# Performance work log

Measured on AMD Instinct MI355X. Metric: run time of the kernel, lower is better.

Reference implementation:

```python
import jax, jax.numpy as jnp
import numpy as np

N_NODES = 50000
N_EDGES = 400000
NODE_DIM = 128
EDGE_DIM = 64
MSG_DIM = 128
EPS = 1e-5


def _linear_init(key, out_f, in_f):
    kw, kb = jax.random.split(key)
    bound = 1.0 / np.sqrt(in_f)
    W = jax.random.uniform(kw, (out_f, in_f), jnp.float32, -bound, bound)
    b = jax.random.uniform(kb, (out_f,), jnp.float32, -bound, bound)
    return W, b


def setup_inputs() -> dict:
    key = jax.random.key(0)
    ks = jax.random.split(key, 10)
    node_features = jax.random.normal(ks[0], (N_NODES, NODE_DIM), jnp.float32)
    edge_features = jax.random.normal(ks[1], (N_EDGES, EDGE_DIM), jnp.float32)
    edge_indices = jax.random.randint(ks[2], (2, N_EDGES), 0, N_NODES, jnp.int64 if jax.config.jax_enable_x64 else jnp.int32)
    cat_dim = 2 * NODE_DIM + EDGE_DIM  # 320
    Wm1, bm1 = _linear_init(ks[3], MSG_DIM, cat_dim)
    Wm2, bm2 = _linear_init(ks[4], MSG_DIM, MSG_DIM)
    Wm3, bm3 = _linear_init(ks[5], MSG_DIM, MSG_DIM)
    We1, be1 = _linear_init(ks[6], EDGE_DIM, cat_dim)
    We2, be2 = _linear_init(ks[7], EDGE_DIM, EDGE_DIM)
    Wn, bn = _linear_init(ks[8], NODE_DIM, NODE_DIM + MSG_DIM)
    gamma = jnp.ones((NODE_DIM,), jnp.float32)
    beta = jnp.zeros((NODE_DIM,), jnp.float32)
    return {
        'node_features': node_features,
        'edge_features': edge_features,
        'edge_indices': edge_indices,
        'Wm1': Wm1, 'bm1': bm1, 'Wm2': Wm2, 'bm2': bm2, 'Wm3': Wm3, 'bm3': bm3,
        'We1': We1, 'be1': be1, 'We2': We2, 'be2': be2,
        'Wn': Wn, 'bn': bn, 'gamma': gamma, 'beta': beta,
    }


def reference(node_features, edge_features, edge_indices,
              Wm1, bm1, Wm2, bm2, Wm3, bm3,
              We1, be1, We2, be2,
              Wn, bn, gamma, beta):
    src, dst = edge_indices[0], edge_indices[1]
    # [E, 2*node_dim + edge_dim]: gathered endpoints + edge feature
    h = jnp.concatenate([node_features[src], node_features[dst], edge_features], axis=-1)
    # message MLP: Linear-ReLU-Linear-ReLU-Linear
    m = jax.nn.relu(h @ Wm1.T + bm1)
    m = jax.nn.relu(m @ Wm2.T + bm2)
    m = m @ Wm3.T + bm3  # [E, msg_dim]
    # scatter-add messages to destination nodes
    messages = jax.ops.segment_sum(m, dst, num_segments=node_features.shape[0])
    # edge update MLP: Linear-ReLU-Linear
    e = jax.nn.relu(h @ We1.T + be1)
    updated_edges = e @ We2.T + be2
    # node update: Linear-ReLU-LayerNorm
    u = jax.nn.relu(jnp.concatenate([node_features, messages], axis=-1) @ Wn.T + bn)
    mu = jnp.mean(u, axis=-1, keepdims=True)
    var = jnp.mean(jnp.square(u - mu), axis=-1, keepdims=True)
    updated_nodes = (u - mu) * jax.lax.rsqrt(var + EPS) * gamma + beta
    return updated_nodes, updated_edges
```

## Files before the change

### kernel.cpp

```cpp
#include <hip/hip_runtime.h>

#define N_EDGES 400000
#define N_NODES 50000
#define ND 128
#define ED 64
#define MD 128
#define CAT 320
#define ET 64
#define MPITCH 136
#define EPITCH 72
#define H2PITCH 264

typedef unsigned short u16;
typedef __attribute__((ext_vector_type(8))) short bf16x8;
typedef __attribute__((ext_vector_type(4))) float f32x4;

#define WS_WM1 0
#define WS_WM2 40960
#define WS_WM3 57344
#define WS_WE1 73728
#define WS_WE2 94208
#define WS_WN  98304
#define WS_WEND 131072
#define WS_NFB 131072
#define WS_FULL_BYTES (2u * (WS_NFB + N_NODES * ND))

__device__ __forceinline__ u16 f2bf(float f) {
  unsigned int x = __float_as_uint(f);
  unsigned int r = (x + 0x7fffu + ((x >> 16) & 1u)) >> 16;
  return (u16)r;
}
__device__ __forceinline__ bf16x8 ld8f(const float* p) {
  f32x4 a = *(const f32x4*)p;
  f32x4 b = *(const f32x4*)(p + 4);
  bf16x8 r;
  r[0] = (short)f2bf(a[0]); r[1] = (short)f2bf(a[1]);
  r[2] = (short)f2bf(a[2]); r[3] = (short)f2bf(a[3]);
  r[4] = (short)f2bf(b[0]); r[5] = (short)f2bf(b[1]);
  r[6] = (short)f2bf(b[2]); r[7] = (short)f2bf(b[3]);
  return r;
}
template<bool WB>
__device__ __forceinline__ bf16x8 ldw(const void* w, size_t off) {
  if (WB) return *(const bf16x8*)((const u16*)w + off);
  else    return ld8f((const float*)w + off);
}
__device__ __forceinline__ int clampi(int v, int hi) {
  v = v < 0 ? 0 : v;
  return v >= hi ? hi - 1 : v;
}

__global__ __launch_bounds__(256) void prep_weights(
    const float* __restrict__ Wm1, const float* __restrict__ Wm2,
    const float* __restrict__ Wm3, const float* __restrict__ We1,
    const float* __restrict__ We2, const float* __restrict__ Wn,
    u16* __restrict__ ws)
{
  int i = blockIdx.x * 256 + threadIdx.x;
  if (i >= WS_WEND) return;
  const float* s; int off;
  if      (i < WS_WM2) { s = Wm1; off = WS_WM1; }
  else if (i < WS_WM3) { s = Wm2; off = WS_WM2; }
  else if (i < WS_WE1) { s = Wm3; off = WS_WM3; }
  else if (i < WS_WE2) { s = We1; off = WS_WE1; }
  else if (i < WS_WN)  { s = We2; off = WS_WE2; }
  else                 { s = Wn;  off = WS_WN;  }
  ws[i] = f2bf(s[i - off]);
}

__global__ __launch_bounds__(256) void prep_nf(
    const float* __restrict__ nf, u16* __restrict__ nfb)
{
  size_t t = ((size_t)blockIdx.x * 256 + threadIdx.x) * 8;
  if (t >= (size_t)N_NODES * ND) return;
  *(bf16x8*)(nfb + t) = ld8f(nf + t);
}

__device__ __forceinline__ void load_indices(
    int* sIdx, int* sFlag, const void* idxRaw, int eb, int tid)
{
  if (tid < ET) {
    unsigned w = ((const unsigned*)idxRaw)[2u * (unsigned)(eb + tid) + 1u];
    int any32 = __any(w != 0u);
    if (tid == 0) *sFlag = any32;
  }
  __syncthreads();
  const bool is32 = (*sFlag != 0);
  if (tid < ET) {
    int v = is32 ? ((const int*)idxRaw)[eb + tid]
                 : (int)((const long long*)idxRaw)[eb + tid];
    sIdx[tid] = clampi(v, N_NODES);
  } else if (tid < 2 * ET) {
    int t = tid - ET;
    int v = is32 ? ((const int*)idxRaw)[N_EDGES + eb + t]
                 : (int)((const long long*)idxRaw)[(size_t)N_EDGES + eb + t];
    sIdx[tid] = clampi(v, N_NODES);
  }
  __syncthreads();
}

template<bool WB, bool NB>
__global__ __launch_bounds__(256, 4) void edge_fused_kernel(
    const float* __restrict__ nf, const u16* __restrict__ nfb,
    const float* __restrict__ ef, const void* __restrict__ idxRaw,
    const void* __restrict__ wm1, const float* __restrict__ bm1,
    const void* __restrict__ wm2, const float* __restrict__ bm2,
    const void* __restrict__ wm3, const float* __restrict__ bm3,
    const void* __restrict__ we1, const float* __restrict__ be1,
    const void* __restrict__ we2, const float* __restrict__ be2,
    float* __restrict__ msg, float* __restrict__ outE)
{
  __shared__ __align__(16) u16 sH[ET * 256];
  __shared__ int sIdx[2 * ET];
  __shared__ int sFlag;
  u16* sM = sH;
  u16* sE1 = sH + ET * MPITCH;

  const int tid  = threadIdx.x;
  const int lane = tid & 63;
  const int wave = tid >> 6;
  const int l15  = lane & 15;
  const int quad = lane >> 4;
  const int eb   = blockIdx.x * ET;

  load_indices(sIdx, &sFlag, idxRaw, eb, tid);

#pragma unroll
  for (int i = 0; i < 8; ++i) {
    int g = i * 256 + tid;
    int e = g >> 5;
    int c = g & 31;
    int node = sIdx[(c < 16) ? e : (ET + e)];
    int cc = c & 15;
    bf16x8 v;
    if (NB) v = *(const bf16x8*)(nfb + (size_t)node * ND + cc * 8);
    else    v = ld8f(nf + (size_t)node * ND + cc * 8);
    int pc = c ^ (e & 7);
    *(bf16x8*)&sH[e * 256 + pc * 8] = v;
  }
  __syncthreads();

  f32x4 acc1[3][4] = {};
  for (int kk = 0; kk < 10; ++kk) {
    int ko = kk * 32 + quad * 8;
    bf16x8 a[4];
#pragma unroll
    for (int m = 0; m < 4; ++m) {
      int e = m * 16 + l15;
      if (kk < 8) {
        int cc = ko >> 3;
        a[m] = *(const bf16x8*)&sH[e * 256 + ((cc ^ (e & 7)) * 8)];
      } else {
        a[m] = ld8f(ef + (size_t)(eb + e) * ED + (ko - 256));
      }
    }
#pragma unroll
    for (int i = 0; i < 3; ++i) {
      int nt = 3 * wave + i;
      int f = nt * 16 + l15;
      bf16x8 b = (nt < 8) ? ldw<WB>(wm1, (size_t)f * CAT + ko)
                          : ldw<WB>(we1, (size_t)(f - ND) * CAT + ko);
#pragma unroll
      for (int m = 0; m < 4; ++m)
        acc1[i][m] = __builtin_amdgcn_mfma_f32_16x16x32_bf16(a[m], b, acc1[i][m], 0, 0, 0);
    }
  }
  __syncthreads();

#pragma unroll
  for (int i = 0; i < 3; ++i) {
    int nt = 3 * wave + i;
    int f = nt * 16 + l15;
    float bias = (nt < 8) ? bm1[f] : be1[f - ND];
#pragma unroll
    for (int m = 0; m < 4; ++m)
#pragma unroll
      for (int r = 0; r < 4; ++r) {
        int row = m * 16 + quad * 4 + r;
        float v = acc1[i][m][r] + bias;
        v = v > 0.f ? v : 0.f;
        if (nt < 8) sM[row * MPITCH + f] = f2bf(v);
        else        sE1[row * EPITCH + (f - ND)] = f2bf(v);
      }
  }
  __syncthreads();

  {
    f32x4 acc[4] = {};
    const int f = wave * 16 + l15;
    for (int kk = 0; kk < 2; ++kk) {
      int ko = kk * 32 + quad * 8;
      bf16x8 b = ldw<WB>(we2, (size_t)f * ED + ko);
#pragma unroll
      for (int m = 0; m < 4; ++m) {
        bf16x8 a = *(const bf16x8*)&sE1[(m * 16 + l15) * EPITCH + ko];
        acc[m] = __builtin_amdgcn_mfma_f32_16x16x32_bf16(a, b, acc[m], 0, 0, 0);
      }
    }
    float bias = be2[f];
#pragma unroll
    for (int m = 0; m < 4; ++m)
#pragma unroll
      for (int r = 0; r < 4; ++r) {
        int row = m * 16 + quad * 4 + r;
        outE[(size_t)(eb + row) * ED + f] = acc[m][r] + bias;
      }
  }

  f32x4 acc2[2][4] = {};
  for (int kk = 0; kk < 4; ++kk) {
    int ko = kk * 32 + quad * 8;
    bf16x8 a[4];
#pragma unroll
    for (int m = 0; m < 4; ++m)
      a[m] = *(const bf16x8*)&sM[(m * 16 + l15) * MPITCH + ko];
#pragma unroll
    for (int i = 0; i < 2; ++i) {
      int f = (2 * wave + i) * 16 + l15;
      bf16x8 b = ldw<WB>(wm2, (size_t)f * MD + ko);
#pragma unroll
      for (int m = 0; m < 4; ++m)
        acc2[i][m] = __builtin_amdgcn_mfma_f32_16x16x32_bf16(a[m], b, acc2[i][m], 0, 0, 0);
    }
  }
  __syncthreads();

#pragma unroll
  for (int i = 0; i < 2; ++i) {
    int f = (2 * wave + i) * 16 + l15;
    float bias = bm2[f];
#pragma unroll
    for (int m = 0; m < 4; ++m)
#pragma unroll
      for (int r = 0; r < 4; ++r) {
        int row = m * 16 + quad * 4 + r;
        float v = acc2[i][m][r] + bias;
        sM[row * MPITCH + f] = f2bf(v > 0.f ? v : 0.f);
      }
  }
  __syncthreads();

  f32x4 acc3[2][4] = {};
  for (int kk = 0; kk < 4; ++kk) {
    int ko = kk * 32 + quad * 8;
    bf16x8 a[4];
#pragma unroll
    for (int m = 0; m < 4; ++m)
      a[m] = *(const bf16x8*)&sM[(m * 16 + l15) * MPITCH + ko];
#pragma unroll
    for (int i = 0; i < 2; ++i) {
      int f = (2 * wave + i) * 16 + l15;
      bf16x8 b = ldw<WB>(wm3, (size_t)f * MD + ko);
#pragma unroll
      for (int m = 0; m < 4; ++m)
        acc3[i][m] = __builtin_amdgcn_mfma_f32_16x16x32_bf16(a[m], b, acc3[i][m], 0, 0, 0);
    }
  }
#pragma unroll
  for (int i = 0; i < 2; ++i) {
    int f = (2 * wave + i) * 16 + l15;
    float bias = bm3[f];
#pragma unroll
    for (int m = 0; m < 4; ++m)
#pragma unroll
      for (int r = 0; r < 4; ++r) {
        int row = m * 16 + quad * 4 + r;
        int d = sIdx[ET + row];
        atomicAdd(&msg[(size_t)d * MD + f], acc3[i][m][r] + bias);
      }
  }
}

template<bool WB, bool NB>
__global__ __launch_bounds__(256, 4) void node_kernel(
    const float* __restrict__ nf, const u16* __restrict__ nfb,
    const float* __restrict__ msg,
    const void* __restrict__ wn, const float* __restrict__ bn,
    const float* __restrict__ gamma, const float* __restrict__ beta,
    float* __restrict__ outN)
{
  __shared__ __align__(16) u16 sH[ET * H2PITCH];
  __shared__ float sPart[4][ET][2];

  const int tid  = threadIdx.x;
  const int lane = tid & 63;
  const int wave = tid >> 6;
  const int l15  = lane & 15;
  const int quad = lane >> 4;
  const int nb   = blockIdx.x * ET;

#pragma unroll
  for (int i = 0; i < 8; ++i) {
    int g = i * 256 + tid;
    int r = g >> 5;
    int c = g & 31;
    int node = nb + r;
    bool valid = node < N_NODES;
    bf16x8 v = {};
    if (c < 16) {
      if (valid) {
        if (NB) v = *(const bf16x8*)(nfb + (size_t)node * ND + c * 8);
        else    v = ld8f(nf + (size_t)node * ND + c * 8);
      }
      *(bf16x8*)&sH[r * H2PITCH + c * 8] = v;
    } else {
      int co = (c - 16) * 8;
      if (valid) v = ld8f(msg + (size_t)node * MD + co);
      *(bf16x8*)&sH[r * H2PITCH + ND + co] = v;
    }
  }
  __syncthreads();

  f32x4 acc[2][4] = {};
  for (int kk = 0; kk < 8; ++kk) {
    int ko = kk * 32 + quad * 8;
    bf16x8 a[4];
#pragma unroll
    for (int m = 0; m < 4; ++m)
      a[m] = *(const bf16x8*)&sH[(m * 16 + l15) * H2PITCH + ko];
#pragma unroll
    for (int i = 0; i < 2; ++i) {
      int f = (2 * wave + i) * 16 + l15;
      bf16x8 b = ldw<WB>(wn, (size_t)f * 256 + ko);
#pragma unroll
      for (int m = 0; m < 4; ++m)
        acc[i][m] = __builtin_amdgcn_mfma_f32_16x16x32_bf16(a[m], b, acc[i][m], 0, 0, 0);
    }
  }

#pragma unroll
  for (int i = 0; i < 2; ++i) {
    int f = (2 * wave + i) * 16 + l15;
    float bias = bn[f];
#pragma unroll
    for (int m = 0; m < 4; ++m)
#pragma unroll
      for (int r = 0; r < 4; ++r) {
        float v = acc[i][m][r] + bias;
        acc[i][m][r] = v > 0.f ? v : 0.f;
      }
  }

#pragma unroll
  for (int m = 0; m < 4; ++m)
#pragma unroll
    for (int r = 0; r < 4; ++r) {
      float p = acc[0][m][r] + acc[1][m][r];
      float q = acc[0][m][r] * acc[0][m][r] + acc[1][m][r] * acc[1][m][r];
#pragma unroll
      for (int mk = 1; mk < 16; mk <<= 1) {
        p += __shfl_xor(p, mk);
        q += __shfl_xor(q, mk);
      }
      if (l15 == 0) {
        int row = m * 16 + quad * 4 + r;
        sPart[wave][row][0] = p;
        sPart[wave][row][1] = q;
      }
    }
  __syncthreads();

#pragma unroll
  for (int m = 0; m < 4; ++m)
#pragma unroll
    for (int r = 0; r < 4; ++r) {
      int row = m * 16 + quad * 4 + r;
      float ts  = sPart[0][row][0] + sPart[1][row][0] + sPart[2][row][0] + sPart[3][row][0];
      float tss = sPart[0][row][1] + sPart[1][row][1] + sPart[2][row][1] + sPart[3][row][1];
      float mu  = ts * 0.0078125f;
      float var = tss * 0.0078125f - mu * mu;
      var = var > 0.f ? var : 0.f;
      float rstd = rsqrtf(var + 1e-5f);
      int node = nb + row;
      if (node < N_NODES) {
#pragma unroll
        for (int i = 0; i < 2; ++i) {
          int f = (2 * wave + i) * 16 + l15;
          float o = (acc[i][m][r] - mu) * rstd * gamma[f] + beta[f];
          outN[(size_t)node * ND + f] = o;
        }
      }
    }
}

extern "C" void kernel_launch(void* const* d_in, const int* in_sizes, int n_in,
                              void* d_out, int out_size, void* d_ws, size_t ws_size,
                              hipStream_t stream)
{
  const float* nf  = (const float*)d_in[0];
  const float* ef  = (const float*)d_in[1];
  const void*  ei  = d_in[2];
  const float* Wm1 = (const float*)d_in[3];
  const float* bm1 = (const float*)d_in[4];
  const float* Wm2 = (const float*)d_in[5];
  const float* bm2 = (const float*)d_in[6];
  const float* Wm3 = (const float*)d_in[7];
  const float* bm3 = (const float*)d_in[8];
  const float* We1 = (const float*)d_in[9];
  const float* be1 = (const float*)d_in[10];
  const float* We2 = (const float*)d_in[11];
  const float* be2 = (const float*)d_in[12];
  const float* Wn  = (const float*)d_in[13];
  const float* bn  = (const float*)d_in[14];
  const float* gamma = (const float*)d_in[15];
  const float* beta  = (const float*)d_in[16];

  float* outN = (float*)d_out;
  float* outE = outN + (size_t)N_NODES * ND;
  float* msg  = outN;

  const bool haveW  = ws_size >= (size_t)(2u * WS_WEND);
  const bool haveNF = ws_size >= (size_t)WS_FULL_BYTES;
  u16* ws = (u16*)d_ws;
  const u16* nfb = ws + WS_NFB;

  hipMemsetAsync(msg, 0, (size_t)N_NODES * MD * sizeof(float), stream);

  if (haveW) {
    prep_weights<<<(WS_WEND + 255) / 256, 256, 0, stream>>>(
        Wm1, Wm2, Wm3, We1, We2, Wn, ws);
    if (haveNF)
      prep_nf<<<(N_NODES * ND / 8 + 255) / 256, 256, 0, stream>>>(nf, ws + WS_NFB);
  }

  const int egrid = N_EDGES / ET;
  const int ngrid = (N_NODES + ET - 1) / ET;

  if (haveW && haveNF) {
    edge_fused_kernel<true, true><<<egrid, 256, 0, stream>>>(
        nf, nfb, ef, ei,
        ws + WS_WM1, bm1, ws + WS_WM2, bm2, ws + WS_WM3, bm3,
        ws + WS_WE1, be1, ws + WS_WE2, be2, msg, outE);
    node_kernel<true, true><<<ngrid, 256, 0, stream>>>(
        nf, nfb, msg, ws + WS_WN, bn, gamma, beta, outN);
  } else if (haveW) {
    edge_fused_kernel<true, false><<<egrid, 256, 0, stream>>>(
        nf, nullptr, ef, ei,
        ws + WS_WM1, bm1, ws + WS_WM2, bm2, ws + WS_WM3, bm3,
        ws + WS_WE1, be1, ws + WS_WE2, be2, msg, outE);
    node_kernel<true, false><<<ngrid, 256, 0, stream>>>(
        nf, nullptr, msg, ws + WS_WN, bn, gamma, beta, outN);
  } else {
    edge_fused_kernel<false, false><<<egrid, 256, 0, stream>>>(
        nf, nullptr, ef, ei,
        Wm1, bm1, Wm2, bm2, Wm3, bm3, We1, be1, We2, be2, msg, outE);
    node_kernel<false, false><<<ngrid, 256, 0, stream>>>(
        nf, nullptr, msg, Wn, bn, gamma, beta, outN);
  }
}
```

Measured before the change: 532.8 us.

## Drop shared index staging and barriers in edge kernel, shrink node tile

In the edge kernel, edge indices are now read straight from global memory per thread rather than staged in shared memory, which removes two barriers and the shared index arrays. The index-width detection now uses only the first 64 entries, read by each wave. The edge kernel's occupancy hint rises from 4 to 5 blocks per CU. The node kernel moves to 32-node tiles with an occupancy hint of 6, giving more blocks and less shared memory per block. The risks are redundant global index loads, register spills under the tighter launch bounds, and weights reloaded across twice as many node blocks.

```diff
diff --git a/kernel.cpp b/kernel.cpp
--- a/kernel.cpp
+++ b/kernel.cpp
@@ -7,6 +7,7 @@
 #define MD 128
 #define CAT 320
 #define ET 64
+#define NT 32
 #define MPITCH 136
 #define EPITCH 72
 #define H2PITCH 264
@@ -48,6 +49,14 @@
 __device__ __forceinline__ int clampi(int v, int hi) {
   v = v < 0 ? 0 : v;
   return v >= hi ? hi - 1 : v;
+}
+__device__ __forceinline__ bool detect32(const void* idxRaw, int lane) {
+  unsigned w = ((const unsigned*)idxRaw)[2 * lane + 1];
+  return __any(w != 0u) != 0;
+}
+__device__ __forceinline__ int ldidx(const void* idxRaw, bool is32, size_t pos) {
+  return is32 ? ((const int*)idxRaw)[pos]
+              : (int)((const long long*)idxRaw)[pos];
 }
 
 __global__ __launch_bounds__(256) void prep_weights(
@@ -76,31 +85,8 @@
   *(bf16x8*)(nfb + t) = ld8f(nf + t);
 }
 
-__device__ __forceinline__ void load_indices(
-    int* sIdx, int* sFlag, const void* idxRaw, int eb, int tid)
-{
-  if (tid < ET) {
-    unsigned w = ((const unsigned*)idxRaw)[2u * (unsigned)(eb + tid) + 1u];
-    int any32 = __any(w != 0u);
-    if (tid == 0) *sFlag = any32;
-  }
-  __syncthreads();
-  const bool is32 = (*sFlag != 0);
-  if (tid < ET) {
-    int v = is32 ? ((const int*)idxRaw)[eb + tid]
-                 : (int)((const long long*)idxRaw)[eb + tid];
-    sIdx[tid] = clampi(v, N_NODES);
-  } else if (tid < 2 * ET) {
-    int t = tid - ET;
-    int v = is32 ? ((const int*)idxRaw)[N_EDGES + eb + t]
-                 : (int)((const long long*)idxRaw)[(size_t)N_EDGES + eb + t];
-    sIdx[tid] = clampi(v, N_NODES);
-  }
-  __syncthreads();
-}
-
 template<bool WB, bool NB>
-__global__ __launch_bounds__(256, 4) void edge_fused_kernel(
+__global__ __launch_bounds__(256, 5) void edge_fused_kernel(
     const float* __restrict__ nf, const u16* __restrict__ nfb,
     const float* __restrict__ ef, const void* __restrict__ idxRaw,
     const void* __restrict__ wm1, const float* __restrict__ bm1,
@@ -111,8 +97,6 @@
     float* __restrict__ msg, float* __restrict__ outE)
 {
   __shared__ __align__(16) u16 sH[ET * 256];
-  __shared__ int sIdx[2 * ET];
-  __shared__ int sFlag;
   u16* sM = sH;
   u16* sE1 = sH + ET * MPITCH;
 
@@ -123,14 +107,15 @@
   const int quad = lane >> 4;
   const int eb   = blockIdx.x * ET;
 
-  load_indices(sIdx, &sFlag, idxRaw, eb, tid);
+  const bool is32 = detect32(idxRaw, lane);
 
 #pragma unroll
   for (int i = 0; i < 8; ++i) {
     int g = i * 256 + tid;
     int e = g >> 5;
     int c = g & 31;
-    int node = sIdx[(c < 16) ? e : (ET + e)];
+    size_t pos = (c < 16) ? (size_t)(eb + e) : ((size_t)N_EDGES + eb + e);
+    int node = clampi(ldidx(idxRaw, is32, pos), N_NODES);
     int cc = c & 15;
     bf16x8 v;
     if (NB) v = *(const bf16x8*)(nfb + (size_t)node * ND + cc * 8);
@@ -257,40 +242,39 @@
     }
   }
 #pragma unroll
-  for (int i = 0; i < 2; ++i) {
-    int f = (2 * wave + i) * 16 + l15;
-    float bias = bm3[f];
-#pragma unroll
-    for (int m = 0; m < 4; ++m)
-#pragma unroll
-      for (int r = 0; r < 4; ++r) {
-        int row = m * 16 + quad * 4 + r;
-        int d = sIdx[ET + row];
-        atomicAdd(&msg[(size_t)d * MD + f], acc3[i][m][r] + bias);
-      }
-  }
+  for (int m = 0; m < 4; ++m)
+#pragma unroll
+    for (int r = 0; r < 4; ++r) {
+      int row = m * 16 + quad * 4 + r;
+      int d = clampi(ldidx(idxRaw, is32, (size_t)N_EDGES + eb + row), N_NODES);
+#pragma unroll
+      for (int i = 0; i < 2; ++i) {
+        int f = (2 * wave + i) * 16 + l15;
+        atomicAdd(&msg[(size_t)d * MD + f], acc3[i][m][r] + bm3[f]);
+      }
+    }
 }
 
 template<bool WB, bool NB>
-__global__ __launch_bounds__(256, 4) void node_kernel(
+__global__ __launch_bounds__(256, 6) void node_kernel(
     const float* __restrict__ nf, const u16* __restrict__ nfb,
     const float* __restrict__ msg,
     const void* __restrict__ wn, const float* __restrict__ bn,
     const float* __restrict__ gamma, const float* __restrict__ beta,
     float* __restrict__ outN)
 {
-  __shared__ __align__(16) u16 sH[ET * H2PITCH];
-  __shared__ float sPart[4][ET][2];
+  __shared__ __align__(16) u16 sH[NT * H2PITCH];
+  __shared__ float sPart[4][NT][2];
 
   const int tid  = threadIdx.x;
   const int lane = tid & 63;
   const int wave = tid >> 6;
   const int l15  = lane & 15;
   const int quad = lane >> 4;
-  const int nb   = blockIdx.x * ET;
-
-#pragma unroll
-  for (int i = 0; i < 8; ++i) {
+  const int nb   = blockIdx.x * NT;
+
+#pragma unroll
+  for (int i = 0; i < 4; ++i) {
     int g = i * 256 + tid;
     int r = g >> 5;
     int c = g & 31;
@@ -311,19 +295,19 @@
   }
   __syncthreads();
 
-  f32x4 acc[2][4] = {};
+  f32x4 acc[2][2] = {};
   for (int kk = 0; kk < 8; ++kk) {
     int ko = kk * 32 + quad * 8;
-    bf16x8 a[4];
-#pragma unroll
-    for (int m = 0; m < 4; ++m)
+    bf16x8 a[2];
+#pragma unroll
+    for (int m = 0; m < 2; ++m)
       a[m] = *(const bf16x8*)&sH[(m * 16 + l15) * H2PITCH + ko];
 #pragma unroll
     for (int i = 0; i < 2; ++i) {
       int f = (2 * wave + i) * 16 + l15;
       bf16x8 b = ldw<WB>(wn, (size_t)f * 256 + ko);
 #pragma unroll
-      for (int m = 0; m < 4; ++m)
+      for (int m = 0; m < 2; ++m)
         acc[i][m] = __builtin_amdgcn_mfma_f32_16x16x32_bf16(a[m], b, acc[i][m], 0, 0, 0);
     }
   }
@@ -333,7 +317,7 @@
     int f = (2 * wave + i) * 16 + l15;
     float bias = bn[f];
 #pragma unroll
-    for (int m = 0; m < 4; ++m)
+    for (int m = 0; m < 2; ++m)
 #pragma unroll
       for (int r = 0; r < 4; ++r) {
         float v = acc[i][m][r] + bias;
@@ -342,7 +326,7 @@
   }
 
 #pragma unroll
-  for (int m = 0; m < 4; ++m)
+  for (int m = 0; m < 2; ++m)
 #pragma unroll
     for (int r = 0; r < 4; ++r) {
       float p = acc[0][m][r] + acc[1][m][r];
@@ -361,7 +345,7 @@
   __syncthreads();
 
 #pragma unroll
-  for (int m = 0; m < 4; ++m)
+  for (int m = 0; m < 2; ++m)
 #pragma unroll
     for (int r = 0; r < 4; ++r) {
       int row = m * 16 + quad * 4 + r;
@@ -424,7 +408,7 @@
   }
 
   const int egrid = N_EDGES / ET;
-  const int ngrid = (N_NODES + ET - 1) / ET;
+  const int ngrid = (N_NODES + NT - 1) / NT;
 
   if (haveW && haveNF) {
     edge_fused_kernel<true, true><<<egrid, 256, 0, stream>>>(
```

Result: slower. 690.5 us (+29.6%).
